# Performance work log

Measured on AMD Instinct MI355X. Metric: run time of the kernel, lower is better.

The kernel has to match this reference:

```python
import jax, jax.numpy as jnp
import numpy as np

# Grid derived from defaults: pc_range=(0,-40,-3,70.4,40,1), voxel=(0.2,0.2,4)
GX, GY = 352, 400          # round((70.4-0)/0.2), round((40-(-40))/0.2)
B, P = 4, 65536            # samples, points per sample
NSEG = B * GX * GY + 1     # dense pillar-id space + 1 sentinel for masked points
OUT_CH = 64
BN_EPS = 1e-3


def setup_inputs() -> dict:
    key = jax.random.key(0)
    k1, k2, k3 = jax.random.split(key, 3)
    xyz_min = jnp.array([0.0, -40.0, -3.0], jnp.float32)
    xyz_max = jnp.array([70.4, 40.0, 1.0], jnp.float32)
    xyz = jax.random.uniform(k1, (B, P, 3), jnp.float32, minval=xyz_min, maxval=xyz_max)
    rest = jax.random.normal(k2, (B, P, 4), jnp.float32)  # rcs, v_r, v_r_comp, time
    points = jnp.concatenate([xyz, rest], axis=-1)        # [B, P, 7]
    W = jax.random.normal(k3, (OUT_CH, 13), jnp.float32) * (1.0 / np.sqrt(13.0))
    gamma = jnp.ones((OUT_CH,), jnp.float32)
    beta = jnp.zeros((OUT_CH,), jnp.float32)
    return {"points": points, "W": W, "gamma": gamma, "beta": beta}


def reference(points, W, gamma, beta):
    Bn, Pn, _ = points.shape
    pts = points.reshape(Bn * Pn, 7)                      # [N, 7] (= torch points[:, 1:])
    dtype = pts.dtype
    voxel = jnp.array([0.2, 0.2, 4.0], dtype)
    pc_min = jnp.array([0.0, -40.0, -3.0], dtype)
    batch_idx = jnp.repeat(jnp.arange(Bn, dtype=jnp.int32), Pn)

    coords_f = (pts[:, :3] - pc_min) / voxel              # float voxel coords
    mask = ((coords_f[:, 0] >= 0) & (coords_f[:, 0] < GX)
            & (coords_f[:, 1] >= 0) & (coords_f[:, 1] < GY))
    coords = coords_f.astype(jnp.int32)                   # [N, 3] (cx, cy, cz)
    sentinel = Bn * GX * GY                               # trash segment for masked points
    lin = jnp.where(mask,
                    batch_idx * (GX * GY) + coords[:, 0] * GY + coords[:, 1],
                    sentinel)
    # torch.unique(..., return_inverse=True, dim=0) on (batch, cx, cy) rows ==
    # unique of the bijective linear id (same sorted order).
    unq, unq_inv = jnp.unique(lin, return_inverse=True, size=NSEG, fill_value=sentinel)

    cnt = jax.ops.segment_sum(jnp.ones((lin.shape[0], 1), dtype), unq_inv, num_segments=NSEG)
    mean_xyz = jax.ops.segment_sum(pts[:, :3], unq_inv, num_segments=NSEG) / jnp.maximum(cnt, 1.0)
    f_cluster = pts[:, :3] - mean_xyz[unq_inv]
    f_center = pts[:, :3] - (coords.astype(dtype) * voxel + voxel * 0.5 + pc_min)
    feats = jnp.concatenate([pts, f_cluster, f_center], axis=-1)   # [N, 13]

    # PFN layer (last_layer=True): Linear -> BN1d (training stats) -> ReLU
    x = feats @ W.T                                       # [N, 64]
    mu = x.mean(axis=0)
    var = x.var(axis=0)                                   # biased, as BN training
    x = jax.nn.relu((x - mu) * jax.lax.rsqrt(var + BN_EPS) * gamma + beta)

    fmax = jax.ops.segment_max(x, unq_inv, num_segments=NSEG)     # scatter_max
    x_max = fmax[unq_inv]                                 # gather back (PFN output)
    feat_max = jax.ops.segment_max(x_max, unq_inv, num_segments=NSEG)

    valid = (unq < sentinel)[:, None]                     # real pillars only
    feat_max = jnp.where(valid, feat_max, 0.0)            # padded/empty -> 0

    b = unq // (GX * GY)
    rem = unq % (GX * GY)
    cx = rem // GY
    cy = rem % GY
    coords_out = jnp.stack([b, cy, cx], axis=1).astype(jnp.int32)  # (batch, y, x)
    grid_size = jnp.array([GY, GX], jnp.int32)
    return feat_max, coords_out, grid_size
```

## Files before the change

kernel.cpp:

```cpp
#include <hip/hip_runtime.h>
#include <stdint.h>
#include <utility>

#define NPTS   262144
#define GXGY   140800
#define GYv    400
#define NSEG   563201
#define SENT   563200
#define NB_SCAN 275
#define PIL_BLOCKS 2048
#define CNT_BLOCKS 512
#define PC_BLOCKS  512

constexpr size_t alignup(size_t x) { return (x + 255) & ~(size_t)255; }
constexpr size_t O_CNT  = 0;
constexpr size_t O_MOM  = alignup(O_CNT + (size_t)NSEG * 4);
constexpr size_t O_DONE = alignup(O_MOM + 104 * 4);
constexpr size_t ZERO_BYTES = alignup(O_DONE + 256);
constexpr size_t O_PPTR = ZERO_BYTES;
constexpr size_t O_ROWI = alignup(O_PPTR + (size_t)NSEG * 4);
constexpr size_t O_FEAT = alignup(O_ROWI + (size_t)NPTS * 16);
constexpr size_t O_BSO  = alignup(O_FEAT + (size_t)NPTS * 32);
constexpr size_t O_BSC  = alignup(O_BSO + NB_SCAN * 4);
constexpr size_t O_KP   = alignup(O_BSC + NB_SCAN * 4);
constexpr size_t O_WF   = alignup(O_KP + 256);
constexpr size_t O_SH   = alignup(O_WF + 832 * 4);

__device__ __forceinline__ int point_lin(float x, float y, int b, bool& mask) {
  float cxf = x / 0.2f;
  float cyf = (y + 40.0f) / 0.2f;
  int cx = (int)cxf, cy = (int)cyf;
  mask = (cxf >= 0.0f) && (cxf < 352.0f) && (cyf >= 0.0f) && (cyf < 400.0f);
  return mask ? (b * GXGY + cx * GYv + cy) : SENT;
}

__global__ __launch_bounds__(256) void k_count(const float* __restrict__ pts,
                                               unsigned int* __restrict__ cnt,
                                               float* __restrict__ mom) {
  int tid = threadIdx.x;
  float acc[65];
#pragma unroll
  for (int u = 0; u < 65; u++) acc[u] = 0.f;

  for (int rep = 0; rep < 2; rep++) {
    int i = rep * (CNT_BLOCKS * 256) + blockIdx.x * 256 + tid;
    const float* p = pts + (size_t)i * 7;
    float x = p[0], y = p[1], z = p[2];
    float w3 = p[3], w4 = p[4], w5 = p[5], w6 = p[6];
    bool m;
    int lin = point_lin(x, y, i >> 16, m);
    atomicAdd(&cnt[lin], 1u);
    int cx = (int)(x / 0.2f);
    int cy = (int)((y + 40.0f) / 0.2f);
    int cz = (int)((z + 3.0f) / 4.0f);
    float g[10] = {x, y, z, w3, w4, w5, w6,
                   x - ((float)cx * 0.2f + 0.1f + 0.0f),
                   y - ((float)cy * 0.2f + 0.1f - 40.0f),
                   z - ((float)cz * 4.0f + 2.0f - 3.0f)};
#pragma unroll
    for (int q = 0; q < 10; q++) acc[q] += g[q];
    int idx = 10;
#pragma unroll
    for (int pp = 0; pp < 10; pp++)
#pragma unroll
      for (int q = pp; q < 10; q++) { acc[idx] += g[pp] * g[q]; idx++; }
  }

  __shared__ float red[4][65];
  int wv = tid >> 6, lane = tid & 63;
#pragma unroll
  for (int u = 0; u < 65; u++) {
    float v = acc[u];
    v += __shfl_xor(v, 1);  v += __shfl_xor(v, 2);  v += __shfl_xor(v, 4);
    v += __shfl_xor(v, 8);  v += __shfl_xor(v, 16); v += __shfl_xor(v, 32);
    if (lane == 0) red[wv][u] = v;
  }
  __syncthreads();
  int t = tid;
  if (t < 104 && !(t >= 7 && t <= 9)) {
    int rix;
    if (t < 13) {
      rix = (t < 7) ? t : t - 3;
    } else {
      int u2 = t - 13, j = 0;
      while (u2 >= 13 - j) { u2 -= 13 - j; j++; }
      int k = j + u2;
      int a = (j < 7) ? j : (j < 10 ? j - 7 : j - 3);
      int b = (k < 7) ? k : (k < 10 ? k - 7 : k - 3);
      int lo = a < b ? a : b, hi = a < b ? b : a;
      rix = 10 + lo * (21 - lo) / 2 + (hi - lo);
    }
    atomicAdd(&mom[t], red[0][rix] + red[1][rix] + red[2][rix] + red[3][rix]);
  }
}

__global__ __launch_bounds__(256) void k_scan1(const unsigned int* __restrict__ cnt,
                                               unsigned int* __restrict__ bso,
                                               unsigned int* __restrict__ bsc) {
  int t = threadIdx.x;
  int base = blockIdx.x * 2048 + t * 8;
  const uint4* c4 = (const uint4*)(cnt + base);
  uint4 a = c4[0], b = c4[1];
  unsigned so = (a.x > 0) + (a.y > 0) + (a.z > 0) + (a.w > 0) +
                (b.x > 0) + (b.y > 0) + (b.z > 0) + (b.w > 0);
  unsigned sc = a.x + a.y + a.z + a.w + b.x + b.y + b.z + b.w;
  for (int m = 1; m < 64; m <<= 1) { so += __shfl_xor(so, m); sc += __shfl_xor(sc, m); }
  __shared__ unsigned wo[4], wc[4];
  if ((t & 63) == 0) { wo[t >> 6] = so; wc[t >> 6] = sc; }
  __syncthreads();
  if (t == 0) {
    bso[blockIdx.x] = wo[0] + wo[1] + wo[2] + wo[3];
    bsc[blockIdx.x] = wc[0] + wc[1] + wc[2] + wc[3];
  }
}

__global__ __launch_bounds__(256) void k_scan3(const unsigned int* __restrict__ cnt,
                                               const unsigned int* __restrict__ bso,
                                               const unsigned int* __restrict__ bsc,
                                               uint4* __restrict__ rowinfo,
                                               unsigned int* __restrict__ pptr,
                                               unsigned int* __restrict__ kp) {
  int t = threadIdx.x;
  unsigned vo_m = 0, vc_m = 0, vo_a = 0;
  for (int e = t; e < NB_SCAN; e += 256) {
    unsigned o = bso[e], c = bsc[e];
    vo_a += o;
    if (e < (int)blockIdx.x) { vo_m += o; vc_m += c; }
  }
  for (int m = 1; m < 64; m <<= 1) {
    vo_m += __shfl_xor(vo_m, m);
    vc_m += __shfl_xor(vc_m, m);
    vo_a += __shfl_xor(vo_a, m);
  }
  __shared__ unsigned s0[4], s1[4], s2[4];
  int wv = t >> 6;
  if ((t & 63) == 0) { s0[wv] = vo_m; s1[wv] = vc_m; s2[wv] = vo_a; }
  __syncthreads();
  unsigned boo = s0[0] + s0[1] + s0[2] + s0[3];
  unsigned boc = s1[0] + s1[1] + s1[2] + s1[3];
  unsigned tot = s2[0] + s2[1] + s2[2] + s2[3];
  if (blockIdx.x == 0 && t == 0) *kp = tot;

  int base = blockIdx.x * 2048 + t * 8;
  const uint4* q = (const uint4*)(cnt + base);
  uint4 a = q[0], b = q[1];
  unsigned c[8] = {a.x, a.y, a.z, a.w, b.x, b.y, b.z, b.w};
  unsigned po[8], pc[8];
  unsigned so = 0, sc = 0;
#pragma unroll
  for (int k = 0; k < 8; k++) {
    po[k] = so; pc[k] = sc;
    so += (c[k] > 0); sc += c[k];
  }
  __shared__ unsigned sdo[256], sdc[256];
  __syncthreads();
  sdo[t] = so; sdc[t] = sc;
  __syncthreads();
  for (int off = 1; off < 256; off <<= 1) {
    unsigned ao = (t >= off) ? sdo[t - off] : 0u;
    unsigned ac = (t >= off) ? sdc[t - off] : 0u;
    __syncthreads();
    sdo[t] += ao; sdc[t] += ac;
    __syncthreads();
  }
  unsigned eo = sdo[t] - so + boo;
  unsigned ec = sdc[t] - sc + boc;
#pragma unroll
  for (int k = 0; k < 8; k++) {
    if (c[k] > 0) {
      unsigned r = eo + po[k];
      unsigned start = ec + pc[k];
      rowinfo[r] = make_uint4((unsigned)(base + k), start, c[k], 0u);
      pptr[base + k] = start;
    }
  }
}

__global__ __launch_bounds__(256) void k_sortfeat(const float* __restrict__ pts,
                                                  unsigned int* __restrict__ pptr,
                                                  float* __restrict__ feat) {
  int i = blockIdx.x * 256 + threadIdx.x;
  if (i >= NPTS) return;
  const float* p = pts + (size_t)i * 7;
  float x = p[0], y = p[1], z = p[2];
  bool m;
  int lin = point_lin(x, y, i >> 16, m);
  if (lin == SENT) return;
  unsigned pos = atomicAdd(&pptr[lin], 1u);
  float4* fb = (float4*)(feat + (size_t)pos * 8);
  fb[0] = make_float4(x, y, z, p[3]);
  fb[1] = make_float4(p[4], p[5], p[6], 0.0f);
}

__global__ __launch_bounds__(256) void k_pilcorr(const uint4* __restrict__ rowinfo,
                                                 const float* __restrict__ feat,
                                                 const unsigned int* __restrict__ kpp,
                                                 float* __restrict__ mom,
                                                 unsigned int* __restrict__ done,
                                                 const float* __restrict__ W,
                                                 const float* __restrict__ g,
                                                 const float* __restrict__ bta,
                                                 float* __restrict__ wf,
                                                 float* __restrict__ sh) {
  int tid = threadIdx.x;
  unsigned kp = *kpp;
  float cS1[3] = {0.f, 0.f, 0.f};
  float cAH[30], cUU[6];
#pragma unroll
  for (int u = 0; u < 30; u++) cAH[u] = 0.f;
#pragma unroll
  for (int u = 0; u < 6; u++) cUU[u] = 0.f;

  for (unsigned r = blockIdx.x * 256 + tid; r < kp; r += PC_BLOCKS * 256) {
    uint4 ri = rowinfo[r];
    unsigned start = ri.y, n = ri.z;
    const float4* fp = (const float4*)(feat + (size_t)start * 8);
    float S[10];
#pragma unroll
    for (int u = 0; u < 10; u++) S[u] = 0.f;
    for (unsigned p = 0; p < n; p++) {
      float4 A = fp[2 * p], Bq = fp[2 * p + 1];
      float x = A.x, y = A.y, z = A.z;
      int cx = (int)(x / 0.2f);
      int cy = (int)((y + 40.0f) / 0.2f);
      int cz = (int)((z + 3.0f) / 4.0f);
      S[0] += x; S[1] += y; S[2] += z; S[3] += A.w;
      S[4] += Bq.x; S[5] += Bq.y; S[6] += Bq.z;
      S[7] += x - ((float)cx * 0.2f + 0.1f + 0.0f);
      S[8] += y - ((float)cy * 0.2f + 0.1f - 40.0f);
      S[9] += z - ((float)cz * 4.0f + 2.0f - 3.0f);
    }
    float fn = (float)n;
    float mm[3] = {S[0] / fn, S[1] / fn, S[2] / fn};
    cS1[0] += S[0] - fn * mm[0];
    cS1[1] += S[1] - fn * mm[1];
    cS1[2] += S[2] - fn * mm[2];
#pragma unroll
    for (int a = 0; a < 3; a++)
#pragma unroll
      for (int h = 0; h < 10; h++) cAH[a * 10 + h] += mm[a] * S[h];
    int e = 0;
#pragma unroll
    for (int a = 0; a < 3; a++)
#pragma unroll
      for (int b = a; b < 3; b++) { cUU[e] += mm[a] * S[b]; e++; }
  }

  float vals[39];
#pragma unroll
  for (int u = 0; u < 3; u++)  vals[u] = cS1[u];
#pragma unroll
  for (int u = 0; u < 30; u++) vals[3 + u] = cAH[u];
#pragma unroll
  for (int u = 0; u < 6; u++)  vals[33 + u] = cUU[u];

  __shared__ float red[4][39];
  int wv = tid >> 6, lane = tid & 63;
#pragma unroll
  for (int u = 0; u < 39; u++) {
    float v = vals[u];
    v += __shfl_xor(v, 1);  v += __shfl_xor(v, 2);  v += __shfl_xor(v, 4);
    v += __shfl_xor(v, 8);  v += __shfl_xor(v, 16); v += __shfl_xor(v, 32);
    if (lane == 0) red[wv][u] = v;
  }
  __syncthreads();
  if (tid < 39) {
    float v = red[0][tid] + red[1][tid] + red[2][tid] + red[3][tid];
    int slot; float sign;
    if (tid < 3) {
      slot = 7 + tid; sign = 1.f;
    } else if (tid < 33) {
      int a = (tid - 3) / 10, h = (tid - 3) % 10;
      int hf = (h < 7) ? h : h + 3;
      int j = hf < 7 + a ? hf : 7 + a;
      int k = hf < 7 + a ? 7 + a : hf;
      slot = 13 + j * (27 - j) / 2 + (k - j);
      sign = -1.f;
    } else {
      int e = tid - 33;
      int a = (e < 3) ? 0 : (e < 5 ? 1 : 2);
      int b = (e < 3) ? e : (e < 5 ? e - 2 : 2);
      int j = 7 + a, k = 7 + b;
      slot = 13 + j * (27 - j) / 2 + (k - j);
      sign = -1.f;
    }
    atomicAdd(&mom[slot], sign * v);
  }

  __threadfence();
  __syncthreads();
  __shared__ unsigned lastf;
  if (tid == 0) lastf = (atomicAdd(done, 1u) == PC_BLOCKS - 1);
  __syncthreads();
  if (lastf) {
    __shared__ float smom[104];
    for (int u = tid; u < 104; u += 256) smom[u] = atomicAdd(&mom[u], 0.0f);
    __syncthreads();
    if (tid < 64) {
      int c = tid;
      float w[13];
#pragma unroll
      for (int j = 0; j < 13; j++) w[j] = W[c * 13 + j];
      const float invN = 1.0f / (float)NPTS;
      float mu = 0.f;
#pragma unroll
      for (int j = 0; j < 13; j++) mu += w[j] * (smom[j] * invN);
      float e2 = 0.f;
      int mi = 13;
#pragma unroll
      for (int j = 0; j < 13; j++) {
#pragma unroll
        for (int k = j; k < 13; k++) {
          float coef = (j == k) ? 1.0f : 2.0f;
          e2 += coef * w[j] * w[k] * smom[mi];
          mi++;
        }
      }
      e2 *= invN;
      float var = e2 - mu * mu;
      float rsig = 1.0f / sqrtf(var + 1e-3f);
      float sc = g[c] * rsig;
#pragma unroll
      for (int j = 0; j < 13; j++) wf[c * 13 + j] = w[j] * sc;
      sh[c] = bta[c] - mu * sc;
    }
  }
}

__global__ __launch_bounds__(256) void k_pillar(const float* __restrict__ wf,
                                                const float* __restrict__ sh,
                                                const uint4* __restrict__ rowinfo,
                                                const unsigned int* __restrict__ kp_p,
                                                const float* __restrict__ feat,
                                                float* __restrict__ out) {
  int tid = threadIdx.x;
  int lane = tid & 15;
  int ch0 = lane * 4;
  float wr[52];
  float shv[4], wx[4], wy[4], wz[4];
#pragma unroll
  for (int c4 = 0; c4 < 4; c4++) {
    shv[c4] = sh[ch0 + c4];
#pragma unroll
    for (int j = 0; j < 13; j++) wr[c4 * 13 + j] = wf[(ch0 + c4) * 13 + j];
    wx[c4] = wr[c4 * 13 + 0] + wr[c4 * 13 + 7] + wr[c4 * 13 + 10];
    wy[c4] = wr[c4 * 13 + 1] + wr[c4 * 13 + 8] + wr[c4 * 13 + 11];
    wz[c4] = wr[c4 * 13 + 2] + wr[c4 * 13 + 9];
  }
  unsigned kp = *kp_p;

  const int NGRP = PIL_BLOCKS * 16;
  for (int r = blockIdx.x * 16 + (tid >> 4); r < NSEG; r += NGRP) {
    float m0 = -3.4e38f, m1 = -3.4e38f, m2 = -3.4e38f, m3 = -3.4e38f;
    int b = 4, cy = 0, cx = 0;
    if ((unsigned)r < kp) {
      uint4 ri = rowinfo[r];
      unsigned id = ri.x, start = ri.y, n = ri.z;
      b = id / GXGY;
      unsigned rem = id - (unsigned)b * GXGY;
      cx = rem / GYv;
      cy = rem - cx * GYv;
      float gx = (float)cx * 0.2f + 0.1f;
      float gy = (float)cy * 0.2f + 0.1f - 40.0f;
      const float4* fb0 = (const float4*)(feat + (size_t)start * 8);
      float sx = 0.f, sy = 0.f, sz = 0.f;
      for (unsigned p = 0; p < n; p++) {
        float4 A = fb0[2 * p];
        sx += A.x; sy += A.y; sz += A.z;
      }
      float cm = (float)n;
      float mx = sx / cm, my = sy / cm, mz = sz / cm;
      float s0_[4];
#pragma unroll
      for (int c4 = 0; c4 < 4; c4++) {
        s0_[c4] = shv[c4] - wr[c4 * 13 + 7] * mx - wr[c4 * 13 + 8] * my
                          - wr[c4 * 13 + 9] * mz - wr[c4 * 13 + 10] * gx
                          - wr[c4 * 13 + 11] * gy;
      }
      const float4* fb = fb0;
      for (unsigned p = 0; p < n; p++) {
        float4 A = fb[0], Bq = fb[1];
        fb += 2;
        int cz = (int)((A.z + 3.0f) / 4.0f);
        float fz = A.z - ((float)cz * 4.0f + 2.0f - 3.0f);
        float d0, d1, d2, d3;
#define DOT(dst, c4)                                                          \
        dst = s0_[c4];                                                        \
        dst += wx[c4] * A.x;            dst += wy[c4] * A.y;                  \
        dst += wz[c4] * A.z;            dst += wr[c4 * 13 + 3] * A.w;         \
        dst += wr[c4 * 13 + 4] * Bq.x;  dst += wr[c4 * 13 + 5] * Bq.y;        \
        dst += wr[c4 * 13 + 6] * Bq.z;  dst += wr[c4 * 13 + 12] * fz;
        DOT(d0, 0) DOT(d1, 1) DOT(d2, 2) DOT(d3, 3)
#undef DOT
        m0 = fmaxf(m0, d0); m1 = fmaxf(m1, d1);
        m2 = fmaxf(m2, d2); m3 = fmaxf(m3, d3);
      }
    }
    float4 v = make_float4(fmaxf(m0, 0.f), fmaxf(m1, 0.f),
                           fmaxf(m2, 0.f), fmaxf(m3, 0.f));
    *(float4*)(out + (size_t)r * 64 + lane * 4) = v;
    if (lane == 0) {
      float* cc = out + (size_t)NSEG * 64 + (size_t)r * 3;
      cc[0] = (float)b;
      cc[1] = (float)cy;
      cc[2] = (float)cx;
    }
  }
  if (blockIdx.x == 0 && tid == 0) {
    float* g2 = out + (size_t)NSEG * 67;
    g2[0] = 400.0f;
    g2[1] = 352.0f;
  }
}

extern "C" void kernel_launch(void* const* d_in, const int* in_sizes, int n_in,
                              void* d_out, int out_size, void* d_ws, size_t ws_size,
                              hipStream_t stream) {
  const float* pts = (const float*)d_in[0];
  const float* W   = (const float*)d_in[1];
  const float* g   = (const float*)d_in[2];
  const float* bta = (const float*)d_in[3];
  float* out = (float*)d_out;
  char* ws = (char*)d_ws;

  unsigned int* cnt  = (unsigned int*)(ws + O_CNT);
  float*        mom  = (float*)(ws + O_MOM);
  unsigned int* done = (unsigned int*)(ws + O_DONE);
  unsigned int* pptr = (unsigned int*)(ws + O_PPTR);
  uint4*        rowi = (uint4*)(ws + O_ROWI);
  float*        feat = (float*)(ws + O_FEAT);
  unsigned int* bso  = (unsigned int*)(ws + O_BSO);
  unsigned int* bsc  = (unsigned int*)(ws + O_BSC);
  unsigned int* kp   = (unsigned int*)(ws + O_KP);
  float*        wf   = (float*)(ws + O_WF);
  float*        sh   = (float*)(ws + O_SH);
  (void)in_sizes; (void)n_in; (void)out_size; (void)ws_size;

  hipMemsetAsync(ws, 0, ZERO_BYTES, stream);

  k_count   <<<CNT_BLOCKS, 256, 0, stream>>>(pts, cnt, mom);
  k_scan1   <<<NB_SCAN, 256, 0, stream>>>(cnt, bso, bsc);
  k_scan3   <<<NB_SCAN, 256, 0, stream>>>(cnt, bso, bsc, rowi, pptr, kp);
  k_sortfeat<<<NPTS / 256, 256, 0, stream>>>(pts, pptr, feat);
  k_pilcorr <<<PC_BLOCKS, 256, 0, stream>>>(rowi, feat, kp, mom, done, W, g, bta, wf, sh);
  k_pillar  <<<PIL_BLOCKS, 256, 0, stream>>>(wf, sh, rowi, kp, feat, out);
}
```

Baseline: 276.7 us.

## Fuse count, scan, sort and moment kernels into one cooperative kernel

Merges the memset, count, two scan passes, scatter-sort and pillar-correction kernels into a single cooperative launch that uses grid-wide syncs between phases. This removes per-kernel launch gaps, the separate memset, and the last-block-done counter. Per-pillar means are now written to a workspace buffer so the final pillar kernel can read them instead of re-summing the points. The cost is grid.sync overhead, and only 512 blocks stay resident for every phase.

```diff
diff --git a/kernel.cpp b/kernel.cpp
--- a/kernel.cpp
+++ b/kernel.cpp
@@ -1,6 +1,9 @@
 #include <hip/hip_runtime.h>
+#include <hip/hip_cooperative_groups.h>
 #include <stdint.h>
 #include <utility>
+
+namespace cg = cooperative_groups;
 
 #define NPTS   262144
 #define GXGY   140800
@@ -9,18 +12,16 @@
 #define SENT   563200
 #define NB_SCAN 275
 #define PIL_BLOCKS 2048
-#define CNT_BLOCKS 512
-#define PC_BLOCKS  512
+#define CB     512
 
 constexpr size_t alignup(size_t x) { return (x + 255) & ~(size_t)255; }
 constexpr size_t O_CNT  = 0;
 constexpr size_t O_MOM  = alignup(O_CNT + (size_t)NSEG * 4);
-constexpr size_t O_DONE = alignup(O_MOM + 104 * 4);
-constexpr size_t ZERO_BYTES = alignup(O_DONE + 256);
-constexpr size_t O_PPTR = ZERO_BYTES;
+constexpr size_t O_PPTR = alignup(O_MOM + 104 * 4);
 constexpr size_t O_ROWI = alignup(O_PPTR + (size_t)NSEG * 4);
 constexpr size_t O_FEAT = alignup(O_ROWI + (size_t)NPTS * 16);
-constexpr size_t O_BSO  = alignup(O_FEAT + (size_t)NPTS * 32);
+constexpr size_t O_MEAN = alignup(O_FEAT + (size_t)NPTS * 32);
+constexpr size_t O_BSO  = alignup(O_MEAN + (size_t)NPTS * 12);
 constexpr size_t O_BSC  = alignup(O_BSO + NB_SCAN * 4);
 constexpr size_t O_KP   = alignup(O_BSC + NB_SCAN * 4);
 constexpr size_t O_WF   = alignup(O_KP + 256);
@@ -34,267 +35,267 @@
   return mask ? (b * GXGY + cx * GYv + cy) : SENT;
 }
 
-__global__ __launch_bounds__(256) void k_count(const float* __restrict__ pts,
+__global__ __launch_bounds__(256) void k_fused(const float* __restrict__ pts,
                                                unsigned int* __restrict__ cnt,
-                                               float* __restrict__ mom) {
-  int tid = threadIdx.x;
-  float acc[65];
-#pragma unroll
-  for (int u = 0; u < 65; u++) acc[u] = 0.f;
-
-  for (int rep = 0; rep < 2; rep++) {
-    int i = rep * (CNT_BLOCKS * 256) + blockIdx.x * 256 + tid;
-    const float* p = pts + (size_t)i * 7;
-    float x = p[0], y = p[1], z = p[2];
-    float w3 = p[3], w4 = p[4], w5 = p[5], w6 = p[6];
-    bool m;
-    int lin = point_lin(x, y, i >> 16, m);
-    atomicAdd(&cnt[lin], 1u);
-    int cx = (int)(x / 0.2f);
-    int cy = (int)((y + 40.0f) / 0.2f);
-    int cz = (int)((z + 3.0f) / 4.0f);
-    float g[10] = {x, y, z, w3, w4, w5, w6,
-                   x - ((float)cx * 0.2f + 0.1f + 0.0f),
-                   y - ((float)cy * 0.2f + 0.1f - 40.0f),
-                   z - ((float)cz * 4.0f + 2.0f - 3.0f)};
-#pragma unroll
-    for (int q = 0; q < 10; q++) acc[q] += g[q];
-    int idx = 10;
-#pragma unroll
-    for (int pp = 0; pp < 10; pp++)
-#pragma unroll
-      for (int q = pp; q < 10; q++) { acc[idx] += g[pp] * g[q]; idx++; }
-  }
-
-  __shared__ float red[4][65];
-  int wv = tid >> 6, lane = tid & 63;
-#pragma unroll
-  for (int u = 0; u < 65; u++) {
-    float v = acc[u];
-    v += __shfl_xor(v, 1);  v += __shfl_xor(v, 2);  v += __shfl_xor(v, 4);
-    v += __shfl_xor(v, 8);  v += __shfl_xor(v, 16); v += __shfl_xor(v, 32);
-    if (lane == 0) red[wv][u] = v;
-  }
-  __syncthreads();
-  int t = tid;
-  if (t < 104 && !(t >= 7 && t <= 9)) {
-    int rix;
-    if (t < 13) {
-      rix = (t < 7) ? t : t - 3;
-    } else {
-      int u2 = t - 13, j = 0;
-      while (u2 >= 13 - j) { u2 -= 13 - j; j++; }
-      int k = j + u2;
-      int a = (j < 7) ? j : (j < 10 ? j - 7 : j - 3);
-      int b = (k < 7) ? k : (k < 10 ? k - 7 : k - 3);
-      int lo = a < b ? a : b, hi = a < b ? b : a;
-      rix = 10 + lo * (21 - lo) / 2 + (hi - lo);
-    }
-    atomicAdd(&mom[t], red[0][rix] + red[1][rix] + red[2][rix] + red[3][rix]);
-  }
-}
-
-__global__ __launch_bounds__(256) void k_scan1(const unsigned int* __restrict__ cnt,
+                                               float* __restrict__ mom,
                                                unsigned int* __restrict__ bso,
-                                               unsigned int* __restrict__ bsc) {
-  int t = threadIdx.x;
-  int base = blockIdx.x * 2048 + t * 8;
-  const uint4* c4 = (const uint4*)(cnt + base);
-  uint4 a = c4[0], b = c4[1];
-  unsigned so = (a.x > 0) + (a.y > 0) + (a.z > 0) + (a.w > 0) +
-                (b.x > 0) + (b.y > 0) + (b.z > 0) + (b.w > 0);
-  unsigned sc = a.x + a.y + a.z + a.w + b.x + b.y + b.z + b.w;
-  for (int m = 1; m < 64; m <<= 1) { so += __shfl_xor(so, m); sc += __shfl_xor(sc, m); }
-  __shared__ unsigned wo[4], wc[4];
-  if ((t & 63) == 0) { wo[t >> 6] = so; wc[t >> 6] = sc; }
-  __syncthreads();
-  if (t == 0) {
-    bso[blockIdx.x] = wo[0] + wo[1] + wo[2] + wo[3];
-    bsc[blockIdx.x] = wc[0] + wc[1] + wc[2] + wc[3];
-  }
-}
-
-__global__ __launch_bounds__(256) void k_scan3(const unsigned int* __restrict__ cnt,
-                                               const unsigned int* __restrict__ bso,
-                                               const unsigned int* __restrict__ bsc,
+                                               unsigned int* __restrict__ bsc,
                                                uint4* __restrict__ rowinfo,
                                                unsigned int* __restrict__ pptr,
-                                               unsigned int* __restrict__ kp) {
-  int t = threadIdx.x;
-  unsigned vo_m = 0, vc_m = 0, vo_a = 0;
-  for (int e = t; e < NB_SCAN; e += 256) {
-    unsigned o = bso[e], c = bsc[e];
-    vo_a += o;
-    if (e < (int)blockIdx.x) { vo_m += o; vc_m += c; }
-  }
-  for (int m = 1; m < 64; m <<= 1) {
-    vo_m += __shfl_xor(vo_m, m);
-    vc_m += __shfl_xor(vc_m, m);
-    vo_a += __shfl_xor(vo_a, m);
-  }
-  __shared__ unsigned s0[4], s1[4], s2[4];
-  int wv = t >> 6;
-  if ((t & 63) == 0) { s0[wv] = vo_m; s1[wv] = vc_m; s2[wv] = vo_a; }
-  __syncthreads();
-  unsigned boo = s0[0] + s0[1] + s0[2] + s0[3];
-  unsigned boc = s1[0] + s1[1] + s1[2] + s1[3];
-  unsigned tot = s2[0] + s2[1] + s2[2] + s2[3];
-  if (blockIdx.x == 0 && t == 0) *kp = tot;
-
-  int base = blockIdx.x * 2048 + t * 8;
-  const uint4* q = (const uint4*)(cnt + base);
-  uint4 a = q[0], b = q[1];
-  unsigned c[8] = {a.x, a.y, a.z, a.w, b.x, b.y, b.z, b.w};
-  unsigned po[8], pc[8];
-  unsigned so = 0, sc = 0;
-#pragma unroll
-  for (int k = 0; k < 8; k++) {
-    po[k] = so; pc[k] = sc;
-    so += (c[k] > 0); sc += c[k];
-  }
+                                               unsigned int* __restrict__ kp,
+                                               float* __restrict__ feat,
+                                               float* __restrict__ meanr,
+                                               const float* __restrict__ W,
+                                               const float* __restrict__ gam,
+                                               const float* __restrict__ bta,
+                                               float* __restrict__ wf,
+                                               float* __restrict__ shv_out) {
+  cg::grid_group grid = cg::this_grid();
+  int tid = threadIdx.x;
+  int gid = blockIdx.x * 256 + tid;
+  int wv = tid >> 6, lane = tid & 63;
+
+  __shared__ float red65[4][65];
+  __shared__ unsigned s0[4], s1v[4], s2[4];
   __shared__ unsigned sdo[256], sdc[256];
-  __syncthreads();
-  sdo[t] = so; sdc[t] = sc;
-  __syncthreads();
-  for (int off = 1; off < 256; off <<= 1) {
-    unsigned ao = (t >= off) ? sdo[t - off] : 0u;
-    unsigned ac = (t >= off) ? sdc[t - off] : 0u;
-    __syncthreads();
-    sdo[t] += ao; sdc[t] += ac;
-    __syncthreads();
-  }
-  unsigned eo = sdo[t] - so + boo;
-  unsigned ec = sdc[t] - sc + boc;
-#pragma unroll
-  for (int k = 0; k < 8; k++) {
-    if (c[k] > 0) {
-      unsigned r = eo + po[k];
-      unsigned start = ec + pc[k];
-      rowinfo[r] = make_uint4((unsigned)(base + k), start, c[k], 0u);
-      pptr[base + k] = start;
-    }
-  }
-}
-
-__global__ __launch_bounds__(256) void k_sortfeat(const float* __restrict__ pts,
-                                                  unsigned int* __restrict__ pptr,
-                                                  float* __restrict__ feat) {
-  int i = blockIdx.x * 256 + threadIdx.x;
-  if (i >= NPTS) return;
-  const float* p = pts + (size_t)i * 7;
-  float x = p[0], y = p[1], z = p[2];
-  bool m;
-  int lin = point_lin(x, y, i >> 16, m);
-  if (lin == SENT) return;
-  unsigned pos = atomicAdd(&pptr[lin], 1u);
-  float4* fb = (float4*)(feat + (size_t)pos * 8);
-  fb[0] = make_float4(x, y, z, p[3]);
-  fb[1] = make_float4(p[4], p[5], p[6], 0.0f);
-}
-
-__global__ __launch_bounds__(256) void k_pilcorr(const uint4* __restrict__ rowinfo,
-                                                 const float* __restrict__ feat,
-                                                 const unsigned int* __restrict__ kpp,
-                                                 float* __restrict__ mom,
-                                                 unsigned int* __restrict__ done,
-                                                 const float* __restrict__ W,
-                                                 const float* __restrict__ g,
-                                                 const float* __restrict__ bta,
-                                                 float* __restrict__ wf,
-                                                 float* __restrict__ sh) {
-  int tid = threadIdx.x;
-  unsigned kp = *kpp;
-  float cS1[3] = {0.f, 0.f, 0.f};
-  float cAH[30], cUU[6];
-#pragma unroll
-  for (int u = 0; u < 30; u++) cAH[u] = 0.f;
-#pragma unroll
-  for (int u = 0; u < 6; u++) cUU[u] = 0.f;
-
-  for (unsigned r = blockIdx.x * 256 + tid; r < kp; r += PC_BLOCKS * 256) {
-    uint4 ri = rowinfo[r];
-    unsigned start = ri.y, n = ri.z;
-    const float4* fp = (const float4*)(feat + (size_t)start * 8);
-    float S[10];
-#pragma unroll
-    for (int u = 0; u < 10; u++) S[u] = 0.f;
-    for (unsigned p = 0; p < n; p++) {
-      float4 A = fp[2 * p], Bq = fp[2 * p + 1];
-      float x = A.x, y = A.y, z = A.z;
+  __shared__ float red39[4][39];
+  __shared__ float smom[104];
+
+  for (int u = gid; u < NSEG; u += CB * 256) cnt[u] = 0u;
+  if (gid < 104) mom[gid] = 0.f;
+  grid.sync();
+
+  {
+    float acc[65];
+#pragma unroll
+    for (int u = 0; u < 65; u++) acc[u] = 0.f;
+    for (int rep = 0; rep < 2; rep++) {
+      int i = rep * (CB * 256) + gid;
+      const float* p = pts + (size_t)i * 7;
+      float x = p[0], y = p[1], z = p[2];
+      float w3 = p[3], w4 = p[4], w5 = p[5], w6 = p[6];
+      bool m;
+      int lin = point_lin(x, y, i >> 16, m);
+      atomicAdd(&cnt[lin], 1u);
       int cx = (int)(x / 0.2f);
       int cy = (int)((y + 40.0f) / 0.2f);
       int cz = (int)((z + 3.0f) / 4.0f);
-      S[0] += x; S[1] += y; S[2] += z; S[3] += A.w;
-      S[4] += Bq.x; S[5] += Bq.y; S[6] += Bq.z;
-      S[7] += x - ((float)cx * 0.2f + 0.1f + 0.0f);
-      S[8] += y - ((float)cy * 0.2f + 0.1f - 40.0f);
-      S[9] += z - ((float)cz * 4.0f + 2.0f - 3.0f);
-    }
-    float fn = (float)n;
-    float mm[3] = {S[0] / fn, S[1] / fn, S[2] / fn};
-    cS1[0] += S[0] - fn * mm[0];
-    cS1[1] += S[1] - fn * mm[1];
-    cS1[2] += S[2] - fn * mm[2];
-#pragma unroll
-    for (int a = 0; a < 3; a++)
-#pragma unroll
-      for (int h = 0; h < 10; h++) cAH[a * 10 + h] += mm[a] * S[h];
-    int e = 0;
-#pragma unroll
-    for (int a = 0; a < 3; a++)
-#pragma unroll
-      for (int b = a; b < 3; b++) { cUU[e] += mm[a] * S[b]; e++; }
-  }
-
-  float vals[39];
-#pragma unroll
-  for (int u = 0; u < 3; u++)  vals[u] = cS1[u];
-#pragma unroll
-  for (int u = 0; u < 30; u++) vals[3 + u] = cAH[u];
-#pragma unroll
-  for (int u = 0; u < 6; u++)  vals[33 + u] = cUU[u];
-
-  __shared__ float red[4][39];
-  int wv = tid >> 6, lane = tid & 63;
-#pragma unroll
-  for (int u = 0; u < 39; u++) {
-    float v = vals[u];
-    v += __shfl_xor(v, 1);  v += __shfl_xor(v, 2);  v += __shfl_xor(v, 4);
-    v += __shfl_xor(v, 8);  v += __shfl_xor(v, 16); v += __shfl_xor(v, 32);
-    if (lane == 0) red[wv][u] = v;
-  }
-  __syncthreads();
-  if (tid < 39) {
-    float v = red[0][tid] + red[1][tid] + red[2][tid] + red[3][tid];
-    int slot; float sign;
-    if (tid < 3) {
-      slot = 7 + tid; sign = 1.f;
-    } else if (tid < 33) {
-      int a = (tid - 3) / 10, h = (tid - 3) % 10;
-      int hf = (h < 7) ? h : h + 3;
-      int j = hf < 7 + a ? hf : 7 + a;
-      int k = hf < 7 + a ? 7 + a : hf;
-      slot = 13 + j * (27 - j) / 2 + (k - j);
-      sign = -1.f;
-    } else {
-      int e = tid - 33;
-      int a = (e < 3) ? 0 : (e < 5 ? 1 : 2);
-      int b = (e < 3) ? e : (e < 5 ? e - 2 : 2);
-      int j = 7 + a, k = 7 + b;
-      slot = 13 + j * (27 - j) / 2 + (k - j);
-      sign = -1.f;
-    }
-    atomicAdd(&mom[slot], sign * v);
-  }
-
-  __threadfence();
-  __syncthreads();
-  __shared__ unsigned lastf;
-  if (tid == 0) lastf = (atomicAdd(done, 1u) == PC_BLOCKS - 1);
-  __syncthreads();
-  if (lastf) {
-    __shared__ float smom[104];
-    for (int u = tid; u < 104; u += 256) smom[u] = atomicAdd(&mom[u], 0.0f);
+      float g[10] = {x, y, z, w3, w4, w5, w6,
+                     x - ((float)cx * 0.2f + 0.1f + 0.0f),
+                     y - ((float)cy * 0.2f + 0.1f - 40.0f),
+                     z - ((float)cz * 4.0f + 2.0f - 3.0f)};
+#pragma unroll
+      for (int q = 0; q < 10; q++) acc[q] += g[q];
+      int idx = 10;
+#pragma unroll
+      for (int pp = 0; pp < 10; pp++)
+#pragma unroll
+        for (int q = pp; q < 10; q++) { acc[idx] += g[pp] * g[q]; idx++; }
+    }
+#pragma unroll
+    for (int u = 0; u < 65; u++) {
+      float v = acc[u];
+      v += __shfl_xor(v, 1);  v += __shfl_xor(v, 2);  v += __shfl_xor(v, 4);
+      v += __shfl_xor(v, 8);  v += __shfl_xor(v, 16); v += __shfl_xor(v, 32);
+      if (lane == 0) red65[wv][u] = v;
+    }
+    __syncthreads();
+    int t = tid;
+    if (t < 104 && !(t >= 7 && t <= 9)) {
+      int rix;
+      if (t < 13) {
+        rix = (t < 7) ? t : t - 3;
+      } else {
+        int u2 = t - 13, j = 0;
+        while (u2 >= 13 - j) { u2 -= 13 - j; j++; }
+        int k = j + u2;
+        int a = (j < 7) ? j : (j < 10 ? j - 7 : j - 3);
+        int b = (k < 7) ? k : (k < 10 ? k - 7 : k - 3);
+        int lo = a < b ? a : b, hi = a < b ? b : a;
+        rix = 10 + lo * (21 - lo) / 2 + (hi - lo);
+      }
+      atomicAdd(&mom[t], red65[0][rix] + red65[1][rix] + red65[2][rix] + red65[3][rix]);
+    }
+  }
+  grid.sync();
+
+  if (blockIdx.x < NB_SCAN) {
+    int base = blockIdx.x * 2048 + tid * 8;
+    const uint4* c4 = (const uint4*)(cnt + base);
+    uint4 a = c4[0], b = c4[1];
+    unsigned so = (a.x > 0) + (a.y > 0) + (a.z > 0) + (a.w > 0) +
+                  (b.x > 0) + (b.y > 0) + (b.z > 0) + (b.w > 0);
+    unsigned sc = a.x + a.y + a.z + a.w + b.x + b.y + b.z + b.w;
+    for (int m = 1; m < 64; m <<= 1) { so += __shfl_xor(so, m); sc += __shfl_xor(sc, m); }
+    if (lane == 0) { s0[wv] = so; s1v[wv] = sc; }
+    __syncthreads();
+    if (tid == 0) {
+      bso[blockIdx.x] = s0[0] + s0[1] + s0[2] + s0[3];
+      bsc[blockIdx.x] = s1v[0] + s1v[1] + s1v[2] + s1v[3];
+    }
+  }
+  grid.sync();
+
+  if (blockIdx.x < NB_SCAN) {
+    unsigned vo_m = 0, vc_m = 0, vo_a = 0;
+    for (int e = tid; e < NB_SCAN; e += 256) {
+      unsigned o = bso[e], c = bsc[e];
+      vo_a += o;
+      if (e < (int)blockIdx.x) { vo_m += o; vc_m += c; }
+    }
+    for (int m = 1; m < 64; m <<= 1) {
+      vo_m += __shfl_xor(vo_m, m);
+      vc_m += __shfl_xor(vc_m, m);
+      vo_a += __shfl_xor(vo_a, m);
+    }
+    __syncthreads();
+    if (lane == 0) { s0[wv] = vo_m; s1v[wv] = vc_m; s2[wv] = vo_a; }
+    __syncthreads();
+    unsigned boo = s0[0] + s0[1] + s0[2] + s0[3];
+    unsigned boc = s1v[0] + s1v[1] + s1v[2] + s1v[3];
+    unsigned tot = s2[0] + s2[1] + s2[2] + s2[3];
+    if (blockIdx.x == 0 && tid == 0) *kp = tot;
+
+    int base = blockIdx.x * 2048 + tid * 8;
+    const uint4* q = (const uint4*)(cnt + base);
+    uint4 a = q[0], b = q[1];
+    unsigned c[8] = {a.x, a.y, a.z, a.w, b.x, b.y, b.z, b.w};
+    unsigned po[8], pc[8];
+    unsigned so = 0, sc = 0;
+#pragma unroll
+    for (int k = 0; k < 8; k++) {
+      po[k] = so; pc[k] = sc;
+      so += (c[k] > 0); sc += c[k];
+    }
+    sdo[tid] = so; sdc[tid] = sc;
+    __syncthreads();
+    for (int off = 1; off < 256; off <<= 1) {
+      unsigned ao = (tid >= off) ? sdo[tid - off] : 0u;
+      unsigned ac = (tid >= off) ? sdc[tid - off] : 0u;
+      __syncthreads();
+      sdo[tid] += ao; sdc[tid] += ac;
+      __syncthreads();
+    }
+    unsigned eo = sdo[tid] - so + boo;
+    unsigned ec = sdc[tid] - sc + boc;
+#pragma unroll
+    for (int k = 0; k < 8; k++) {
+      if (c[k] > 0) {
+        unsigned r = eo + po[k];
+        unsigned start = ec + pc[k];
+        rowinfo[r] = make_uint4((unsigned)(base + k), start, c[k], 0u);
+        pptr[base + k] = start;
+      }
+    }
+  }
+  grid.sync();
+
+  for (int rep = 0; rep < 2; rep++) {
+    int i = rep * (CB * 256) + gid;
+    const float* p = pts + (size_t)i * 7;
+    float x = p[0], y = p[1], z = p[2];
+    bool m;
+    int lin = point_lin(x, y, i >> 16, m);
+    if (lin != SENT) {
+      unsigned pos = atomicAdd(&pptr[lin], 1u);
+      float4* fb = (float4*)(feat + (size_t)pos * 8);
+      fb[0] = make_float4(x, y, z, p[3]);
+      fb[1] = make_float4(p[4], p[5], p[6], 0.0f);
+    }
+  }
+  grid.sync();
+
+  {
+    unsigned kpv = *kp;
+    float cS1[3] = {0.f, 0.f, 0.f};
+    float cAH[30], cUU[6];
+#pragma unroll
+    for (int u = 0; u < 30; u++) cAH[u] = 0.f;
+#pragma unroll
+    for (int u = 0; u < 6; u++) cUU[u] = 0.f;
+
+    for (unsigned r = blockIdx.x * 256 + tid; r < kpv; r += CB * 256) {
+      uint4 ri = rowinfo[r];
+      unsigned start = ri.y, n = ri.z;
+      const float4* fp = (const float4*)(feat + (size_t)start * 8);
+      float S[10];
+#pragma unroll
+      for (int u = 0; u < 10; u++) S[u] = 0.f;
+      for (unsigned p = 0; p < n; p++) {
+        float4 A = fp[2 * p], Bq = fp[2 * p + 1];
+        float x = A.x, y = A.y, z = A.z;
+        int cx = (int)(x / 0.2f);
+        int cy = (int)((y + 40.0f) / 0.2f);
+        int cz = (int)((z + 3.0f) / 4.0f);
+        S[0] += x; S[1] += y; S[2] += z; S[3] += A.w;
+        S[4] += Bq.x; S[5] += Bq.y; S[6] += Bq.z;
+        S[7] += x - ((float)cx * 0.2f + 0.1f + 0.0f);
+        S[8] += y - ((float)cy * 0.2f + 0.1f - 40.0f);
+        S[9] += z - ((float)cz * 4.0f + 2.0f - 3.0f);
+      }
+      float fn = (float)n;
+      float mm[3] = {S[0] / fn, S[1] / fn, S[2] / fn};
+      meanr[(size_t)r * 3 + 0] = mm[0];
+      meanr[(size_t)r * 3 + 1] = mm[1];
+      meanr[(size_t)r * 3 + 2] = mm[2];
+      cS1[0] += S[0] - fn * mm[0];
+      cS1[1] += S[1] - fn * mm[1];
+      cS1[2] += S[2] - fn * mm[2];
+#pragma unroll
+      for (int a = 0; a < 3; a++)
+#pragma unroll
+        for (int h = 0; h < 10; h++) cAH[a * 10 + h] += mm[a] * S[h];
+      int e = 0;
+#pragma unroll
+      for (int a = 0; a < 3; a++)
+#pragma unroll
+        for (int b = a; b < 3; b++) { cUU[e] += mm[a] * S[b]; e++; }
+    }
+
+    float vals[39];
+#pragma unroll
+    for (int u = 0; u < 3; u++)  vals[u] = cS1[u];
+#pragma unroll
+    for (int u = 0; u < 30; u++) vals[3 + u] = cAH[u];
+#pragma unroll
+    for (int u = 0; u < 6; u++)  vals[33 + u] = cUU[u];
+
+    __syncthreads();
+#pragma unroll
+    for (int u = 0; u < 39; u++) {
+      float v = vals[u];
+      v += __shfl_xor(v, 1);  v += __shfl_xor(v, 2);  v += __shfl_xor(v, 4);
+      v += __shfl_xor(v, 8);  v += __shfl_xor(v, 16); v += __shfl_xor(v, 32);
+      if (lane == 0) red39[wv][u] = v;
+    }
+    __syncthreads();
+    if (tid < 39) {
+      float v = red39[0][tid] + red39[1][tid] + red39[2][tid] + red39[3][tid];
+      int slot; float sign;
+      if (tid < 3) {
+        slot = 7 + tid; sign = 1.f;
+      } else if (tid < 33) {
+        int a = (tid - 3) / 10, h = (tid - 3) % 10;
+        int hf = (h < 7) ? h : h + 3;
+        int j = hf < 7 + a ? hf : 7 + a;
+        int k = hf < 7 + a ? 7 + a : hf;
+        slot = 13 + j * (27 - j) / 2 + (k - j);
+        sign = -1.f;
+      } else {
+        int e = tid - 33;
+        int a = (e < 3) ? 0 : (e < 5 ? 1 : 2);
+        int b = (e < 3) ? e : (e < 5 ? e - 2 : 2);
+        int j = 7 + a, k = 7 + b;
+        slot = 13 + j * (27 - j) / 2 + (k - j);
+        sign = -1.f;
+      }
+      atomicAdd(&mom[slot], sign * v);
+    }
+  }
+  grid.sync();
+
+  if (blockIdx.x == 0) {
+    for (int u = tid; u < 104; u += 256) smom[u] = mom[u];
     __syncthreads();
     if (tid < 64) {
       int c = tid;
@@ -319,10 +320,10 @@
       e2 *= invN;
       float var = e2 - mu * mu;
       float rsig = 1.0f / sqrtf(var + 1e-3f);
-      float sc = g[c] * rsig;
+      float sc = gam[c] * rsig;
 #pragma unroll
       for (int j = 0; j < 13; j++) wf[c * 13 + j] = w[j] * sc;
-      sh[c] = bta[c] - mu * sc;
+      shv_out[c] = bta[c] - mu * sc;
     }
   }
 }
@@ -332,6 +333,7 @@
                                                 const uint4* __restrict__ rowinfo,
                                                 const unsigned int* __restrict__ kp_p,
                                                 const float* __restrict__ feat,
+                                                const float* __restrict__ meanr,
                                                 float* __restrict__ out) {
   int tid = threadIdx.x;
   int lane = tid & 15;
@@ -362,14 +364,9 @@
       cy = rem - cx * GYv;
       float gx = (float)cx * 0.2f + 0.1f;
       float gy = (float)cy * 0.2f + 0.1f - 40.0f;
-      const float4* fb0 = (const float4*)(feat + (size_t)start * 8);
-      float sx = 0.f, sy = 0.f, sz = 0.f;
-      for (unsigned p = 0; p < n; p++) {
-        float4 A = fb0[2 * p];
-        sx += A.x; sy += A.y; sz += A.z;
-      }
-      float cm = (float)n;
-      float mx = sx / cm, my = sy / cm, mz = sz / cm;
+      float mx = meanr[(size_t)r * 3 + 0];
+      float my = meanr[(size_t)r * 3 + 1];
+      float mz = meanr[(size_t)r * 3 + 2];
       float s0_[4];
 #pragma unroll
       for (int c4 = 0; c4 < 4; c4++) {
@@ -377,7 +374,7 @@
                           - wr[c4 * 13 + 9] * mz - wr[c4 * 13 + 10] * gx
                           - wr[c4 * 13 + 11] * gy;
       }
-      const float4* fb = fb0;
+      const float4* fb = (const float4*)(feat + (size_t)start * 8);
       for (unsigned p = 0; p < n; p++) {
         float4 A = fb[0], Bq = fb[1];
         fb += 2;
@@ -418,30 +415,27 @@
                               hipStream_t stream) {
   const float* pts = (const float*)d_in[0];
   const float* W   = (const float*)d_in[1];
-  const float* g   = (const float*)d_in[2];
+  const float* gam = (const float*)d_in[2];
   const float* bta = (const float*)d_in[3];
   float* out = (float*)d_out;
   char* ws = (char*)d_ws;
 
   unsigned int* cnt  = (unsigned int*)(ws + O_CNT);
   float*        mom  = (float*)(ws + O_MOM);
-  unsigned int* done = (unsigned int*)(ws + O_DONE);
   unsigned int* pptr = (unsigned int*)(ws + O_PPTR);
   uint4*        rowi = (uint4*)(ws + O_ROWI);
   float*        feat = (float*)(ws + O_FEAT);
+  float*        mnr  = (float*)(ws + O_MEAN);
   unsigned int* bso  = (unsigned int*)(ws + O_BSO);
   unsigned int* bsc  = (unsigned int*)(ws + O_BSC);
   unsigned int* kp   = (unsigned int*)(ws + O_KP);
   float*        wf   = (float*)(ws + O_WF);
-  float*        sh   = (float*)(ws + O_SH);
+  float*        shb  = (float*)(ws + O_SH);
   (void)in_sizes; (void)n_in; (void)out_size; (void)ws_size;
 
-  hipMemsetAsync(ws, 0, ZERO_BYTES, stream);
-
-  k_count   <<<CNT_BLOCKS, 256, 0, stream>>>(pts, cnt, mom);
-  k_scan1   <<<NB_SCAN, 256, 0, stream>>>(cnt, bso, bsc);
-  k_scan3   <<<NB_SCAN, 256, 0, stream>>>(cnt, bso, bsc, rowi, pptr, kp);
-  k_sortfeat<<<NPTS / 256, 256, 0, stream>>>(pts, pptr, feat);
-  k_pilcorr <<<PC_BLOCKS, 256, 0, stream>>>(rowi, feat, kp, mom, done, W, g, bta, wf, sh);
-  k_pillar  <<<PIL_BLOCKS, 256, 0, stream>>>(wf, sh, rowi, kp, feat, out);
+  void* args[] = {&pts, &cnt, &mom, &bso, &bsc, &rowi, &pptr, &kp,
+                  &feat, &mnr, &W, &gam, &bta, &wf, &shb};
+  hipLaunchCooperativeKernel((const void*)k_fused, dim3(CB), dim3(256),
+                             args, 0, stream);
+  k_pillar<<<PIL_BLOCKS, 256, 0, stream>>>(wf, shb, rowi, kp, feat, mnr, out);
 }
```

Measured after the change: 569.6 us. 2.06x slower.

## Fold block scan counts into count kernel and cache pillar means

Applied to the files above, without the earlier changes.

Removes the separate block-summary scan kernel by having the counting kernel atomically accumulate per-2048-segment point counts and occupied-pillar counts as points are binned. The pillar correction kernel now stores each pillar's xyz mean, so the final pillar kernel reads it instead of re-walking the pillar's points to recompute it. This saves one launch, one pass over the count array and one pass over the sorted features. In exchange it adds two extra global atomics per point on a small, heavily contended array and extra mean-buffer traffic.

```diff
diff --git a/kernel.cpp b/kernel.cpp
--- a/kernel.cpp
+++ b/kernel.cpp
@@ -16,13 +16,14 @@
 constexpr size_t O_CNT  = 0;
 constexpr size_t O_MOM  = alignup(O_CNT + (size_t)NSEG * 4);
 constexpr size_t O_DONE = alignup(O_MOM + 104 * 4);
-constexpr size_t ZERO_BYTES = alignup(O_DONE + 256);
+constexpr size_t O_BSO  = alignup(O_DONE + 256);
+constexpr size_t O_BSC  = alignup(O_BSO + NB_SCAN * 4);
+constexpr size_t ZERO_BYTES = alignup(O_BSC + NB_SCAN * 4);
 constexpr size_t O_PPTR = ZERO_BYTES;
 constexpr size_t O_ROWI = alignup(O_PPTR + (size_t)NSEG * 4);
 constexpr size_t O_FEAT = alignup(O_ROWI + (size_t)NPTS * 16);
-constexpr size_t O_BSO  = alignup(O_FEAT + (size_t)NPTS * 32);
-constexpr size_t O_BSC  = alignup(O_BSO + NB_SCAN * 4);
-constexpr size_t O_KP   = alignup(O_BSC + NB_SCAN * 4);
+constexpr size_t O_MEAN = alignup(O_FEAT + (size_t)NPTS * 32);
+constexpr size_t O_KP   = alignup(O_MEAN + (size_t)NPTS * 12);
 constexpr size_t O_WF   = alignup(O_KP + 256);
 constexpr size_t O_SH   = alignup(O_WF + 832 * 4);
 
@@ -36,6 +37,8 @@
 
 __global__ __launch_bounds__(256) void k_count(const float* __restrict__ pts,
                                                unsigned int* __restrict__ cnt,
+                                               unsigned int* __restrict__ bso,
+                                               unsigned int* __restrict__ bsc,
                                                float* __restrict__ mom) {
   int tid = threadIdx.x;
   float acc[65];
@@ -49,7 +52,11 @@
     float w3 = p[3], w4 = p[4], w5 = p[5], w6 = p[6];
     bool m;
     int lin = point_lin(x, y, i >> 16, m);
-    atomicAdd(&cnt[lin], 1u);
+    unsigned old = atomicAdd(&cnt[lin], 1u);
+    if (lin != SENT) {
+      atomicAdd(&bsc[lin >> 11], 1u);
+      if (old == 0u) atomicAdd(&bso[lin >> 11], 1u);
+    }
     int cx = (int)(x / 0.2f);
     int cy = (int)((y + 40.0f) / 0.2f);
     int cz = (int)((z + 3.0f) / 4.0f);
@@ -91,26 +98,6 @@
       rix = 10 + lo * (21 - lo) / 2 + (hi - lo);
     }
     atomicAdd(&mom[t], red[0][rix] + red[1][rix] + red[2][rix] + red[3][rix]);
-  }
-}
-
-__global__ __launch_bounds__(256) void k_scan1(const unsigned int* __restrict__ cnt,
-                                               unsigned int* __restrict__ bso,
-                                               unsigned int* __restrict__ bsc) {
-  int t = threadIdx.x;
-  int base = blockIdx.x * 2048 + t * 8;
-  const uint4* c4 = (const uint4*)(cnt + base);
-  uint4 a = c4[0], b = c4[1];
-  unsigned so = (a.x > 0) + (a.y > 0) + (a.z > 0) + (a.w > 0) +
-                (b.x > 0) + (b.y > 0) + (b.z > 0) + (b.w > 0);
-  unsigned sc = a.x + a.y + a.z + a.w + b.x + b.y + b.z + b.w;
-  for (int m = 1; m < 64; m <<= 1) { so += __shfl_xor(so, m); sc += __shfl_xor(sc, m); }
-  __shared__ unsigned wo[4], wc[4];
-  if ((t & 63) == 0) { wo[t >> 6] = so; wc[t >> 6] = sc; }
-  __syncthreads();
-  if (t == 0) {
-    bso[blockIdx.x] = wo[0] + wo[1] + wo[2] + wo[3];
-    bsc[blockIdx.x] = wc[0] + wc[1] + wc[2] + wc[3];
   }
 }
 
@@ -196,6 +183,7 @@
                                                  const float* __restrict__ feat,
                                                  const unsigned int* __restrict__ kpp,
                                                  float* __restrict__ mom,
+                                                 float* __restrict__ meanr,
                                                  unsigned int* __restrict__ done,
                                                  const float* __restrict__ W,
                                                  const float* __restrict__ g,
@@ -232,6 +220,9 @@
     }
     float fn = (float)n;
     float mm[3] = {S[0] / fn, S[1] / fn, S[2] / fn};
+    meanr[(size_t)r * 3 + 0] = mm[0];
+    meanr[(size_t)r * 3 + 1] = mm[1];
+    meanr[(size_t)r * 3 + 2] = mm[2];
     cS1[0] += S[0] - fn * mm[0];
     cS1[1] += S[1] - fn * mm[1];
     cS1[2] += S[2] - fn * mm[2];
@@ -332,6 +323,7 @@
                                                 const uint4* __restrict__ rowinfo,
                                                 const unsigned int* __restrict__ kp_p,
                                                 const float* __restrict__ feat,
+                                                const float* __restrict__ meanr,
                                                 float* __restrict__ out) {
   int tid = threadIdx.x;
   int lane = tid & 15;
@@ -362,14 +354,9 @@
       cy = rem - cx * GYv;
       float gx = (float)cx * 0.2f + 0.1f;
       float gy = (float)cy * 0.2f + 0.1f - 40.0f;
-      const float4* fb0 = (const float4*)(feat + (size_t)start * 8);
-      float sx = 0.f, sy = 0.f, sz = 0.f;
-      for (unsigned p = 0; p < n; p++) {
-        float4 A = fb0[2 * p];
-        sx += A.x; sy += A.y; sz += A.z;
-      }
-      float cm = (float)n;
-      float mx = sx / cm, my = sy / cm, mz = sz / cm;
+      float mx = meanr[(size_t)r * 3 + 0];
+      float my = meanr[(size_t)r * 3 + 1];
+      float mz = meanr[(size_t)r * 3 + 2];
       float s0_[4];
 #pragma unroll
       for (int c4 = 0; c4 < 4; c4++) {
@@ -377,7 +364,7 @@
                           - wr[c4 * 13 + 9] * mz - wr[c4 * 13 + 10] * gx
                           - wr[c4 * 13 + 11] * gy;
       }
-      const float4* fb = fb0;
+      const float4* fb = (const float4*)(feat + (size_t)start * 8);
       for (unsigned p = 0; p < n; p++) {
         float4 A = fb[0], Bq = fb[1];
         fb += 2;
@@ -426,11 +413,12 @@
   unsigned int* cnt  = (unsigned int*)(ws + O_CNT);
   float*        mom  = (float*)(ws + O_MOM);
   unsigned int* done = (unsigned int*)(ws + O_DONE);
+  unsigned int* bso  = (unsigned int*)(ws + O_BSO);
+  unsigned int* bsc  = (unsigned int*)(ws + O_BSC);
   unsigned int* pptr = (unsigned int*)(ws + O_PPTR);
   uint4*        rowi = (uint4*)(ws + O_ROWI);
   float*        feat = (float*)(ws + O_FEAT);
-  unsigned int* bso  = (unsigned int*)(ws + O_BSO);
-  unsigned int* bsc  = (unsigned int*)(ws + O_BSC);
+  float*        mnr  = (float*)(ws + O_MEAN);
   unsigned int* kp   = (unsigned int*)(ws + O_KP);
   float*        wf   = (float*)(ws + O_WF);
   float*        sh   = (float*)(ws + O_SH);
@@ -438,10 +426,9 @@
 
   hipMemsetAsync(ws, 0, ZERO_BYTES, stream);
 
-  k_count   <<<CNT_BLOCKS, 256, 0, stream>>>(pts, cnt, mom);
-  k_scan1   <<<NB_SCAN, 256, 0, stream>>>(cnt, bso, bsc);
+  k_count   <<<CNT_BLOCKS, 256, 0, stream>>>(pts, cnt, bso, bsc, mom);
   k_scan3   <<<NB_SCAN, 256, 0, stream>>>(cnt, bso, bsc, rowi, pptr, kp);
   k_sortfeat<<<NPTS / 256, 256, 0, stream>>>(pts, pptr, feat);
-  k_pilcorr <<<PC_BLOCKS, 256, 0, stream>>>(rowi, feat, kp, mom, done, W, g, bta, wf, sh);
-  k_pillar  <<<PIL_BLOCKS, 256, 0, stream>>>(wf, sh, rowi, kp, feat, out);
-}
+  k_pilcorr <<<PC_BLOCKS, 256, 0, stream>>>(rowi, feat, kp, mom, mnr, done, W, g, bta, wf, sh);
+  k_pillar  <<<PIL_BLOCKS, 256, 0, stream>>>(wf, sh, rowi, kp, feat, mnr, out);
+}
```

Result: slower. 409.9 us (+48.1%).
